# Performance work log

Hardware: AMD Instinct MI355X
Metric: run time of the kernel (lower is better)

## Reference

```python
import jax, jax.numpy as jnp
import numpy as np

B, T, N = 4096, 96, 32
E, K, D_MODEL = 4, 2, 32
PATCHES = (8, 6, 4, 12)
DECOMP_KERNELS = (4, 8, 12)
FOURIER_TOPK = 3
NOISE_EPS = 0.01
LOSS_COEF = 1e-4
SQRT2 = float(np.sqrt(2.0))


def _moving_avg(x, k):
    # x: (B, T, N); replicate-pad so output length stays T (stride-1 avg pool)
    pl, pr = (k - 1) // 2, k // 2
    xp = jnp.concatenate([jnp.repeat(x[:, :1], pl, axis=1), x,
                          jnp.repeat(x[:, -1:], pr, axis=1)], axis=1)
    c = jnp.cumsum(xp, axis=1)
    c = jnp.concatenate([jnp.zeros_like(c[:, :1]), c], axis=1)
    return (c[:, k:] - c[:, :-k]) / k


def _fourier_seasonality(x, topk=FOURIER_TOPK):
    # keep top-k amplitude non-DC frequencies per (batch, node) series
    f = jnp.fft.rfft(x, axis=1)                       # (B, F, N)
    amp = jnp.abs(f).at[:, 0].set(0.0)
    kth = -jnp.sort(-amp, axis=1)[:, topk - 1:topk]   # k-th largest amplitude
    mask = (amp >= kth).astype(f.dtype)
    return jnp.fft.irfft(f * mask, n=x.shape[1], axis=1)


def _cv_squared(v):
    return jnp.var(v, ddof=1) / (jnp.mean(v) ** 2 + 1e-10)


def _prob_in_top_k(clean, noisy, std, top_vals, k):
    # top_vals: (B, k+1) descending noisy top values
    std = jnp.maximum(std, 1e-6)
    thr_in = top_vals[:, k:k + 1]        # (k+1)-th value -> threshold if sample is in
    thr_out = top_vals[:, k - 1:k]       # k-th value -> threshold if sample is out
    z_in = jnp.clip((clean - thr_in) / std, -50.0, 50.0)
    z_out = jnp.clip((clean - thr_out) / std, -50.0, 50.0)
    p_in = jnp.clip(0.5 * (1.0 + jax.lax.erf(z_in / SQRT2)), 0.0, 1.0)
    p_out = jnp.clip(0.5 * (1.0 + jax.lax.erf(z_out / SQRT2)), 0.0, 1.0)
    return jnp.where(noisy > thr_in, p_in, p_out)


def _patch_expert(x2, p, w1, b1, w2, b2):
    # per-expert patch MLP: split T into patches of size p, mix within patch
    Bb, Tt, Nn = x2.shape
    xr = x2.reshape(Bb, Tt // p, p, Nn).transpose(0, 1, 3, 2)  # (B, Pn, N, p)
    h = jax.nn.gelu(xr @ w1 + b1)                               # (B, Pn, N, d)
    y = h @ w2 + b2                                             # (B, Pn, N, p)
    return y.transpose(0, 1, 3, 2).reshape(Bb, Tt, Nn)


def _forward(x, noise, w_start, b_start, wg, bg, wn, bn, eparams):
    x2 = x[..., 0]                                              # (B, T, N)
    trend = jnp.mean(jnp.stack([_moving_avg(x2, k) for k in DECOMP_KERNELS]), axis=0)
    season = _fourier_seasonality(x2)
    new_x = x2 + season + trend

    # ---- noisy top-k gating ----
    x_lin = new_x @ w_start + b_start                           # (B, T)
    clean = x_lin @ wg.T + bg                                   # (B, E)
    std = jnp.clip(jax.nn.softplus(x_lin @ wn.T + bn) + NOISE_EPS, 1e-3, 1e3)
    noisy = clean + noise * std
    top_vals, top_idx = jax.lax.top_k(noisy, K + 1)
    gk = jax.nn.softmax(top_vals[:, :K], axis=1)
    rows = jnp.arange(noisy.shape[0])[:, None]
    gates = jnp.zeros_like(noisy).at[rows, top_idx[:, :K]].set(gk)  # (B, E) sparse

    prob = _prob_in_top_k(clean, noisy, std, top_vals, K)
    load = prob.sum(0)
    importance = gates.sum(0)
    balance_loss = (_cv_squared(importance) + _cv_squared(load)) * LOSS_COEF

    # ---- dispatch / expert / combine (dense weighted form; gate==0 rows vanish,
    # same math as SparseDispatcher gather + weighted scatter-add) ----
    out = jnp.zeros_like(x2)
    for i, p in enumerate(PATCHES):
        w1, b1, w2, b2 = eparams[i]
        y = _patch_expert(x2, p, w1, b1, w2, b2)
        out = out + gates[:, i][:, None, None] * y
    return out[..., None], balance_loss


def setup_inputs() -> dict:
    key = jax.random.key(0)
    ks = jax.random.split(key, 32)
    inp = {
        "x": jax.random.normal(ks[0], (B, T, N, 1), jnp.float32),
        "noise": jax.random.normal(ks[1], (B, E), jnp.float32),
        "w_start": 0.1 * jax.random.normal(ks[2], (N,), jnp.float32),
        "b_start": jnp.zeros((1,), jnp.float32),
        "wg": 0.05 * jax.random.normal(ks[3], (E, T), jnp.float32),
        "bg": jnp.zeros((E,), jnp.float32),
        "wn": 0.05 * jax.random.normal(ks[4], (E, T), jnp.float32),
        "bn": jnp.zeros((E,), jnp.float32),
    }
    for i, p in enumerate(PATCHES):
        inp[f"e{i}_w1"] = 0.1 * jax.random.normal(ks[5 + 2 * i], (p, D_MODEL), jnp.float32)
        inp[f"e{i}_b1"] = jnp.zeros((D_MODEL,), jnp.float32)
        inp[f"e{i}_w2"] = 0.1 * jax.random.normal(ks[6 + 2 * i], (D_MODEL, p), jnp.float32)
        inp[f"e{i}_b2"] = jnp.zeros((p,), jnp.float32)
    return inp


def reference(x, noise, w_start, b_start, wg, bg, wn, bn,
              e0_w1, e0_b1, e0_w2, e0_b2,
              e1_w1, e1_b1, e1_w2, e1_b2,
              e2_w1, e2_b1, e2_w2, e2_b2,
              e3_w1, e3_b1, e3_w2, e3_b2):
    eparams = ((e0_w1, e0_b1, e0_w2, e0_b2),
               (e1_w1, e1_b1, e1_w2, e1_b2),
               (e2_w1, e2_b1, e2_w2, e2_b2),
               (e3_w1, e3_b1, e3_w2, e3_b2))
    return _forward(x, noise, w_start, b_start, wg, bg, wn, bn, eparams)
```

## Files before the change

kernel.cpp:

```cpp
#include <hip/hip_runtime.h>
#include <math.h>

#define NTHREADS 256
constexpr int TB = 4096;
constexpr int TT = 96;
constexpr int TN = 32;
constexpr int XLD = 33;

struct Params {
    const float* x; const float* noise;
    const float* w_start; const float* b_start;
    const float* wg; const float* bg; const float* wn; const float* bn;
    const float* ew[16];
    float* out; float* part;
};

__device__ __forceinline__ float gelu_f(float v) {
    float v2 = v * v;
    float u2 = fmaf(0.0713548162726278f * v, v2, 1.5957691216057308f * v);
    float t = __expf(-u2);
    return v * __builtin_amdgcn_rcpf(1.0f + t);
}

template<int P, int L0, int L1, int CB>
__device__ __forceinline__ void patch_acc2(const float* __restrict__ xg,
        const float* __restrict__ w1, const float* __restrict__ w2,
        const float* __restrict__ b1, const float* __restrict__ b2,
        int pbA, int pbB, int n, float g, float (&yA)[12], float (&yB)[12]) {
    float vA[P], vB[P];
    #pragma unroll
    for (int l = 0; l < P; ++l) {
        vA[l] = xg[(pbA * P + l) * TN + n];
        vB[l] = xg[(pbB * P + l) * TN + n];
    }
    #pragma unroll 2
    for (int jb = 0; jb < 8; ++jb) {
        float aA0 = b1[jb * 4 + 0], aA1 = b1[jb * 4 + 1];
        float aA2 = b1[jb * 4 + 2], aA3 = b1[jb * 4 + 3];
        float aB0 = aA0, aB1 = aA1, aB2 = aA2, aB3 = aA3;
        #pragma unroll
        for (int l = 0; l < P; ++l) {
            const float w0 = w1[l * 32 + jb * 4 + 0];
            const float w1v = w1[l * 32 + jb * 4 + 1];
            const float w2v = w1[l * 32 + jb * 4 + 2];
            const float w3 = w1[l * 32 + jb * 4 + 3];
            aA0 = fmaf(vA[l], w0, aA0);  aA1 = fmaf(vA[l], w1v, aA1);
            aA2 = fmaf(vA[l], w2v, aA2); aA3 = fmaf(vA[l], w3, aA3);
            aB0 = fmaf(vB[l], w0, aB0);  aB1 = fmaf(vB[l], w1v, aB1);
            aB2 = fmaf(vB[l], w2v, aB2); aB3 = fmaf(vB[l], w3, aB3);
        }
        float hA[4], hB[4];
        hA[0] = g * gelu_f(aA0); hA[1] = g * gelu_f(aA1);
        hA[2] = g * gelu_f(aA2); hA[3] = g * gelu_f(aA3);
        hB[0] = g * gelu_f(aB0); hB[1] = g * gelu_f(aB1);
        hB[2] = g * gelu_f(aB2); hB[3] = g * gelu_f(aB3);
        #pragma unroll
        for (int l = L0; l < L1; ++l) {
            float accA = yA[CB + l - L0];
            float accB = yB[CB + l - L0];
            #pragma unroll
            for (int q = 0; q < 4; ++q) {
                const float w = w2[(jb * 4 + q) * P + l];
                accA = fmaf(hA[q], w, accA);
                accB = fmaf(hB[q], w, accB);
            }
            yA[CB + l - L0] = accA;
            yB[CB + l - L0] = accB;
        }
    }
    #pragma unroll
    for (int l = L0; l < L1; ++l) {
        yA[CB + l - L0] = fmaf(g, b2[l], yA[CB + l - L0]);
        yB[CB + l - L0] = fmaf(g, b2[l], yB[CB + l - L0]);
    }
}

__global__ __launch_bounds__(NTHREADS) void ams_k1(Params p) {
    __shared__ float xs[TT * XLD];
    __shared__ float ct[96], st[96];
    __shared__ float xlin[96];
    __shared__ float selr[256], seli[256];
    __shared__ int   selk[256];
    __shared__ int   selcnt[32];
    __shared__ float wst[32];
    __shared__ float gtmp[8];
    __shared__ float b0sh;

    const int tid = threadIdx.x;
    const int b = blockIdx.x;

    const float* xb = p.x + (size_t)b * (TT * TN);
    #pragma unroll 1
    for (int idx = tid; idx < TT * TN; idx += NTHREADS)
        xs[(idx >> 5) * XLD + (idx & 31)] = xb[idx];
    if (tid < 96) {
        float ang = (float)tid * 0.06544984694978735f;
        ct[tid] = cosf(ang);
        st[tid] = sinf(ang);
    }
    if (tid < 32) wst[tid] = p.w_start[tid];
    if (tid == 0) b0sh = p.b_start[0];
    __syncthreads();

    {
        const int n = tid >> 3;
        const int kslot = tid & 7;
        const int lane = tid & 63;

        float Sr[12], Si[12];
        #pragma unroll
        for (int bb = 0; bb < 12; ++bb) { Sr[bb] = 0.0f; Si[bb] = 0.0f; }
        {
            const int step = 12 * kslot;
            int idx8 = 0;
            #pragma unroll 2
            for (int a = 0; a < 8; ++a) {
                float c8 = ct[idx8], s8 = st[idx8];
                idx8 += step; idx8 = (idx8 >= 96) ? idx8 - 96 : idx8;
                const float* xrow = &xs[(12 * a) * XLD + n];
                #pragma unroll
                for (int bb = 0; bb < 12; ++bb) {
                    float xv = xrow[bb * XLD];
                    Sr[bb] = fmaf(xv, c8, Sr[bb]);
                    Si[bb] = fmaf(xv, s8, Si[bb]);
                }
            }
        }

        float ar[7], ai[7];
        #pragma unroll
        for (int u = 0; u < 7; ++u) {
            const int k = kslot + 8 * u;
            const float ckv = ct[k];
            const float skv = st[k];
            float cb = 1.0f, sb = 0.0f, arx = 0.0f, aix = 0.0f;
            #pragma unroll
            for (int bb = 0; bb < 12; ++bb) {
                arx = fmaf(cb, Sr[bb], arx);
                arx = fmaf(-sb, Si[bb], arx);
                aix = fmaf(cb, Si[bb], aix);
                aix = fmaf(sb, Sr[bb], aix);
                float cn = fmaf(cb, ckv, -(sb * skv));
                float sn = fmaf(sb, ckv,  cb * skv);
                cb = cn; sb = sn;
            }
            ar[u] = arx; ai[u] = aix;
        }

        float amp[7];
        #pragma unroll
        for (int u = 0; u < 7; ++u) {
            int k = kslot + 8 * u;
            amp[u] = (k == 0) ? 0.0f : ((k <= 48) ? sqrtf(ar[u] * ar[u] + ai[u] * ai[u]) : -1.0f);
        }
        float v1 = -2.0f, v2 = -2.0f, v3 = -2.0f;
        #pragma unroll
        for (int u = 0; u < 7; ++u) {
            float a = amp[u];
            if (a > v1)      { v3 = v2; v2 = v1; v1 = a; }
            else if (a > v2) { v3 = v2; v2 = a; }
            else if (a > v3) { v3 = a; }
        }
        #pragma unroll
        for (int d = 1; d <= 4; d <<= 1) {
            float b1v = __shfl_xor(v1, d, 64);
            float b2v = __shfl_xor(v2, d, 64);
            float b3v = __shfl_xor(v3, d, 64);
            float m1 = fmaxf(v1, b1v), n1 = fminf(v1, b1v);
            float m2 = fmaxf(v2, b2v), n2 = fminf(v2, b2v);
            float s3 = (v1 > b1v) ? v3 : b3v;
            float c3 = fmaxf(fmaxf(fminf(n1, m2), n2), s3);
            v2 = fmaxf(n1, m2);
            v1 = m1;
            v3 = c3;
        }
        int qc = 0;
        #pragma unroll
        for (int u = 0; u < 7; ++u) qc += (amp[u] >= v3) ? 1 : 0;
        int inc = qc;
        #pragma unroll
        for (int d = 1; d <= 4; d <<= 1) {
            int t = __shfl_up(inc, d, 64);
            if (kslot >= d) inc += t;
        }
        int off = inc - qc;
        int cnt = __shfl(inc, lane | 7, 64);
        if (kslot == 0) selcnt[n] = (cnt < 8) ? cnt : 8;
        int w = off;
        #pragma unroll
        for (int u = 0; u < 7; ++u) {
            int k = kslot + 8 * u;
            if (amp[u] >= v3 && w < 8) {
                float wgt = (k == 0 || k == 48) ? (1.0f / 96.0f) : (2.0f / 96.0f);
                selk[w * 32 + n] = k;
                selr[w * 32 + n] = wgt * ar[u];
                seli[w * 32 + n] = wgt * ai[u];
                w++;
            }
        }
    }
    __syncthreads();

    {
        float b0 = b0sh;
        const int t0 = tid >> 5;
        const int n  = tid & 31;
        const int cnt = selcnt[n];
        float A0 = 0, B0 = 0, c0 = 1, s0 = 0, c80 = 1, s80 = 0;
        float A1 = 0, B1 = 0, c1 = 1, s1 = 0, c81 = 1, s81 = 0;
        float A2 = 0, B2 = 0, c2 = 1, s2 = 0, c82 = 1, s82 = 0;
        #define SETROT(Q, A, B, C, S, C8, S8) \
            if (Q < cnt) { \
                int k = selk[Q * 32 + n]; \
                A = selr[Q * 32 + n]; B = seli[Q * 32 + n]; \
                int m0 = (t0 * k) % 96; C = ct[m0]; S = st[m0]; \
                int m8 = (8 * k) % 96;  C8 = ct[m8]; S8 = st[m8]; \
            }
        SETROT(0, A0, B0, c0, s0, c80, s80)
        SETROT(1, A1, B1, c1, s1, c81, s81)
        SETROT(2, A2, B2, c2, s2, c82, s82)
        #undef SETROT
        #pragma unroll 1
        for (int j = 0; j < 12; ++j) {
            int t = t0 + 8 * j;
            float xv = xs[t * XLD + n];
            #define XC(tt) xs[(((tt) < 0) ? 0 : (((tt) > 95) ? 95 : (tt))) * XLD + n]
            float s4  = XC(t - 1) + xv + XC(t + 1) + XC(t + 2);
            float s8  = s4  + XC(t - 3) + XC(t - 2) + XC(t + 3) + XC(t + 4);
            float s12 = s8  + XC(t - 5) + XC(t - 4) + XC(t + 5) + XC(t + 6);
            #undef XC
            float trend = (s4 * 0.25f + s8 * 0.125f + s12 * (1.0f / 12.0f)) * (1.0f / 3.0f);
            float season = A0 * c0 + B0 * s0 + A1 * c1 + B1 * s1 + A2 * c2 + B2 * s2;
            float nc0 = fmaf(c0, c80, -(s0 * s80)), ns0 = fmaf(s0, c80, c0 * s80);
            float nc1 = fmaf(c1, c81, -(s1 * s81)), ns1 = fmaf(s1, c81, c1 * s81);
            float nc2 = fmaf(c2, c82, -(s2 * s82)), ns2 = fmaf(s2, c82, c2 * s82);
            c0 = nc0; s0 = ns0; c1 = nc1; s1 = ns1; c2 = nc2; s2 = ns2;
            #pragma unroll 1
            for (int q = 3; q < cnt; ++q) {
                int k = selk[q * 32 + n];
                int m = (t * k) % 96;
                season = fmaf(selr[q * 32 + n], ct[m], season);
                season = fmaf(seli[q * 32 + n], st[m], season);
            }
            float val = (xv + trend + season) * wst[n];
            #pragma unroll
            for (int d = 16; d >= 1; d >>= 1) val += __shfl_xor(val, d, 64);
            if ((tid & 31) == 0) xlin[t] = val + b0;
        }
    }
    __syncthreads();

    {
        int e8 = tid >> 5;
        int tl = tid & 31;
        int eb = e8 & 3;
        const float* W = ((e8 < 4) ? p.wg : p.wn) + eb * 96;
        float acc = 0.0f;
        #pragma unroll
        for (int c = 0; c < 3; ++c)
            acc = fmaf(xlin[tl + 32 * c], W[tl + 32 * c], acc);
        #pragma unroll
        for (int d = 16; d >= 1; d >>= 1) acc += __shfl_xor(acc, d, 64);
        if (tl == 0) gtmp[e8] = acc + ((e8 < 4) ? p.bg[eb] : p.bn[eb]);
    }
    __syncthreads();
    if (tid == 0) {
        float clean[4], stdv[4], noisy[4];
        #pragma unroll
        for (int e = 0; e < 4; ++e) {
            clean[e] = gtmp[e];
            float r = gtmp[4 + e];
            float sp = fmaxf(r, 0.0f) + log1pf(expf(-fabsf(r)));
            stdv[e] = fminf(fmaxf(sp + 0.01f, 0.001f), 1000.0f);
            noisy[e] = clean[e] + p.noise[(size_t)b * 4 + e] * stdv[e];
        }
        int i1 = 0, i2 = -1;
        float v1 = -INFINITY, v2 = -INFINITY, v3 = -INFINITY;
        for (int e = 0; e < 4; ++e) if (noisy[e] > v1) { v1 = noisy[e]; i1 = e; }
        for (int e = 0; e < 4; ++e) if (e != i1 && noisy[e] > v2) { v2 = noisy[e]; i2 = e; }
        for (int e = 0; e < 4; ++e) if (e != i1 && e != i2 && noisy[e] > v3) { v3 = noisy[e]; }
        float e2 = expf(v2 - v1);
        float g1 = 1.0f / (1.0f + e2);
        float g2 = e2 * g1;
        float gates[4] = {0.0f, 0.0f, 0.0f, 0.0f};
        gates[i1] = g1; gates[i2] = g2;
        const float inv_sqrt2 = 0.7071067811865476f;
        #pragma unroll
        for (int e = 0; e < 4; ++e) {
            float thr = (noisy[e] > v3) ? v3 : v2;
            float z = (clean[e] - thr) / stdv[e];
            z = fminf(fmaxf(z, -50.0f), 50.0f);
            float pr = 0.5f * (1.0f + erff(z * inv_sqrt2));
            pr = fminf(fmaxf(pr, 0.0f), 1.0f);
            p.part[(size_t)b * 8 + e] = gates[e];
            p.part[(size_t)b * 8 + 4 + e] = pr;
        }
    }
}

__global__ __launch_bounds__(NTHREADS) void ams_k2(Params p) {
    const int tid = threadIdx.x;
    const int half = tid >> 7;
    const size_t b = 2 * (size_t)blockIdx.x + half;
    const int g = tid & 127;
    const int cA = ((g >> 5) & 1) * 2 + (g >> 6);
    const int cB = cA + 4;
    const int n = g & 31;

    const float g0 = p.part[b * 8 + 0];
    const float g1 = p.part[b * 8 + 1];
    const float g2 = p.part[b * 8 + 2];
    const float g3 = p.part[b * 8 + 3];
    const float* xg = p.x + b * (TT * TN);

    float yA[12], yB[12];
    #pragma unroll
    for (int r = 0; r < 12; ++r) { yA[r] = 0.0f; yB[r] = 0.0f; }

    if (g0 != 0.0f) {
        if (cA & 1) {
            int pb = (3 * cA - 1) >> 1;
            patch_acc2<8, 4, 8, 0>(xg, p.ew[0], p.ew[2], p.ew[1], p.ew[3], pb,     pb + 6, n, g0, yA, yB);
            patch_acc2<8, 0, 8, 4>(xg, p.ew[0], p.ew[2], p.ew[1], p.ew[3], pb + 1, pb + 7, n, g0, yA, yB);
        } else {
            int pb = (3 * cA) >> 1;
            patch_acc2<8, 0, 8, 0>(xg, p.ew[0], p.ew[2], p.ew[1], p.ew[3], pb,     pb + 6, n, g0, yA, yB);
            patch_acc2<8, 0, 4, 8>(xg, p.ew[0], p.ew[2], p.ew[1], p.ew[3], pb + 1, pb + 7, n, g0, yA, yB);
        }
    }
    if (g1 != 0.0f) {
        patch_acc2<6, 0, 6, 0>(xg, p.ew[4], p.ew[6], p.ew[5], p.ew[7], 2 * cA,     2 * cA + 8, n, g1, yA, yB);
        patch_acc2<6, 0, 6, 6>(xg, p.ew[4], p.ew[6], p.ew[5], p.ew[7], 2 * cA + 1, 2 * cA + 9, n, g1, yA, yB);
    }
    if (g2 != 0.0f) {
        patch_acc2<4, 0, 4, 0>(xg, p.ew[8], p.ew[10], p.ew[9], p.ew[11], 3 * cA,     3 * cA + 12, n, g2, yA, yB);
        patch_acc2<4, 0, 4, 4>(xg, p.ew[8], p.ew[10], p.ew[9], p.ew[11], 3 * cA + 1, 3 * cA + 13, n, g2, yA, yB);
        patch_acc2<4, 0, 4, 8>(xg, p.ew[8], p.ew[10], p.ew[9], p.ew[11], 3 * cA + 2, 3 * cA + 14, n, g2, yA, yB);
    }
    if (g3 != 0.0f) {
        patch_acc2<12, 0, 12, 0>(xg, p.ew[12], p.ew[14], p.ew[13], p.ew[15], cA, cB, n, g3, yA, yB);
    }

    float* ob = p.out + b * (TT * TN);
    float* obA = ob + (size_t)(12 * cA) * 32 + n;
    float* obB = ob + (size_t)(12 * cB) * 32 + n;
    #pragma unroll
    for (int r = 0; r < 12; ++r) {
        obA[r * 32] = yA[r];
        obB[r * 32] = yB[r];
    }
}

__global__ __launch_bounds__(NTHREADS) void ams_finalize(const float* __restrict__ part,
                                                         float* __restrict__ out_loss) {
    __shared__ float red[4][8];
    float acc[8] = {0, 0, 0, 0, 0, 0, 0, 0};
    #pragma unroll 1
    for (int r = threadIdx.x; r < TB; r += NTHREADS) {
        #pragma unroll
        for (int c = 0; c < 8; ++c) acc[c] += part[(size_t)r * 8 + c];
    }
    #pragma unroll
    for (int c = 0; c < 8; ++c) {
        #pragma unroll
        for (int d = 32; d >= 1; d >>= 1) acc[c] += __shfl_xor(acc[c], d, 64);
    }
    int wid = threadIdx.x >> 6;
    if ((threadIdx.x & 63) == 0) {
        #pragma unroll
        for (int c = 0; c < 8; ++c) red[wid][c] = acc[c];
    }
    __syncthreads();
    if (threadIdx.x == 0) {
        float imp[4], load[4];
        #pragma unroll
        for (int c = 0; c < 4; ++c) imp[c]  = red[0][c] + red[1][c] + red[2][c] + red[3][c];
        #pragma unroll
        for (int c = 0; c < 4; ++c) load[c] = red[0][4 + c] + red[1][4 + c] + red[2][4 + c] + red[3][4 + c];
        float mi = (imp[0] + imp[1] + imp[2] + imp[3]) * 0.25f;
        float vi = 0.0f;
        #pragma unroll
        for (int i = 0; i < 4; ++i) { float d = imp[i] - mi; vi += d * d; }
        vi *= (1.0f / 3.0f);
        float ml = (load[0] + load[1] + load[2] + load[3]) * 0.25f;
        float vl = 0.0f;
        #pragma unroll
        for (int i = 0; i < 4; ++i) { float d = load[i] - ml; vl += d * d; }
        vl *= (1.0f / 3.0f);
        float cvi = vi / (mi * mi + 1e-10f);
        float cvl = vl / (ml * ml + 1e-10f);
        out_loss[0] = (cvi + cvl) * 1e-4f;
    }
}

extern "C" void kernel_launch(void* const* d_in, const int* in_sizes, int n_in,
                              void* d_out, int out_size, void* d_ws, size_t ws_size,
                              hipStream_t stream) {
    Params p;
    p.x       = (const float*)d_in[0];
    p.noise   = (const float*)d_in[1];
    p.w_start = (const float*)d_in[2];
    p.b_start = (const float*)d_in[3];
    p.wg      = (const float*)d_in[4];
    p.bg      = (const float*)d_in[5];
    p.wn      = (const float*)d_in[6];
    p.bn      = (const float*)d_in[7];
    for (int i = 0; i < 16; ++i) p.ew[i] = (const float*)d_in[8 + i];
    p.out  = (float*)d_out;
    p.part = (float*)d_ws;

    ams_k1<<<TB, NTHREADS, 0, stream>>>(p);
    ams_k2<<<TB / 2, NTHREADS, 0, stream>>>(p);
    ams_finalize<<<1, NTHREADS, 0, stream>>>((const float*)d_ws,
                                             (float*)d_out + (size_t)TB * TT * TN);
}
```

Measured before the change: 163.7 us.

## Give each k2 thread two 24-step time chunks, loading inputs once into registers

ams_k2 now maps one wavefront per batch row, and each thread owns two 24-step time chunks for one node. 24 is a common multiple of all patch sizes, so every expert's patches line up with chunk boundaries. Each thread loads its 48 input values into registers once and reuses them across all experts. This drops the redundant global loads and the odd/even branching on partial patches. In exchange it doubles per-thread work and register use (48 inputs plus 48 accumulators) and halves the number of threads, which may lower occupancy.

```diff
diff --git a/kernel.cpp b/kernel.cpp
--- a/kernel.cpp
+++ b/kernel.cpp
@@ -22,17 +22,11 @@
     return v * __builtin_amdgcn_rcpf(1.0f + t);
 }
 
-template<int P, int L0, int L1, int CB>
-__device__ __forceinline__ void patch_acc2(const float* __restrict__ xg,
+template<int P, int X0>
+__device__ __forceinline__ void patchF(const float (&x0)[24], const float (&x1)[24],
         const float* __restrict__ w1, const float* __restrict__ w2,
         const float* __restrict__ b1, const float* __restrict__ b2,
-        int pbA, int pbB, int n, float g, float (&yA)[12], float (&yB)[12]) {
-    float vA[P], vB[P];
-    #pragma unroll
-    for (int l = 0; l < P; ++l) {
-        vA[l] = xg[(pbA * P + l) * TN + n];
-        vB[l] = xg[(pbB * P + l) * TN + n];
-    }
+        float g, float (&y0)[24], float (&y1)[24]) {
     #pragma unroll 2
     for (int jb = 0; jb < 8; ++jb) {
         float aA0 = b1[jb * 4 + 0], aA1 = b1[jb * 4 + 1];
@@ -40,14 +34,16 @@
         float aB0 = aA0, aB1 = aA1, aB2 = aA2, aB3 = aA3;
         #pragma unroll
         for (int l = 0; l < P; ++l) {
+            const float vA = x0[X0 + l];
+            const float vB = x1[X0 + l];
             const float w0 = w1[l * 32 + jb * 4 + 0];
             const float w1v = w1[l * 32 + jb * 4 + 1];
             const float w2v = w1[l * 32 + jb * 4 + 2];
             const float w3 = w1[l * 32 + jb * 4 + 3];
-            aA0 = fmaf(vA[l], w0, aA0);  aA1 = fmaf(vA[l], w1v, aA1);
-            aA2 = fmaf(vA[l], w2v, aA2); aA3 = fmaf(vA[l], w3, aA3);
-            aB0 = fmaf(vB[l], w0, aB0);  aB1 = fmaf(vB[l], w1v, aB1);
-            aB2 = fmaf(vB[l], w2v, aB2); aB3 = fmaf(vB[l], w3, aB3);
+            aA0 = fmaf(vA, w0, aA0);  aA1 = fmaf(vA, w1v, aA1);
+            aA2 = fmaf(vA, w2v, aA2); aA3 = fmaf(vA, w3, aA3);
+            aB0 = fmaf(vB, w0, aB0);  aB1 = fmaf(vB, w1v, aB1);
+            aB2 = fmaf(vB, w2v, aB2); aB3 = fmaf(vB, w3, aB3);
         }
         float hA[4], hB[4];
         hA[0] = g * gelu_f(aA0); hA[1] = g * gelu_f(aA1);
@@ -55,23 +51,23 @@
         hB[0] = g * gelu_f(aB0); hB[1] = g * gelu_f(aB1);
         hB[2] = g * gelu_f(aB2); hB[3] = g * gelu_f(aB3);
         #pragma unroll
-        for (int l = L0; l < L1; ++l) {
-            float accA = yA[CB + l - L0];
-            float accB = yB[CB + l - L0];
+        for (int l = 0; l < P; ++l) {
+            float accA = y0[X0 + l];
+            float accB = y1[X0 + l];
             #pragma unroll
             for (int q = 0; q < 4; ++q) {
                 const float w = w2[(jb * 4 + q) * P + l];
                 accA = fmaf(hA[q], w, accA);
                 accB = fmaf(hB[q], w, accB);
             }
-            yA[CB + l - L0] = accA;
-            yB[CB + l - L0] = accB;
+            y0[X0 + l] = accA;
+            y1[X0 + l] = accB;
         }
     }
     #pragma unroll
-    for (int l = L0; l < L1; ++l) {
-        yA[CB + l - L0] = fmaf(g, b2[l], yA[CB + l - L0]);
-        yB[CB + l - L0] = fmaf(g, b2[l], yB[CB + l - L0]);
+    for (int l = 0; l < P; ++l) {
+        y0[X0 + l] = fmaf(g, b2[l], y0[X0 + l]);
+        y1[X0 + l] = fmaf(g, b2[l], y1[X0 + l]);
     }
 }
 
@@ -300,12 +296,10 @@
 
 __global__ __launch_bounds__(NTHREADS) void ams_k2(Params p) {
     const int tid = threadIdx.x;
-    const int half = tid >> 7;
-    const size_t b = 2 * (size_t)blockIdx.x + half;
-    const int g = tid & 127;
-    const int cA = ((g >> 5) & 1) * 2 + (g >> 6);
-    const int cB = cA + 4;
-    const int n = g & 31;
+    const size_t b = 4 * (size_t)blockIdx.x + (tid >> 6);
+    const int lane = tid & 63;
+    const int hi = lane >> 5;
+    const int n = lane & 31;
 
     const float g0 = p.part[b * 8 + 0];
     const float g1 = p.part[b * 8 + 1];
@@ -313,41 +307,51 @@
     const float g3 = p.part[b * 8 + 3];
     const float* xg = p.x + b * (TT * TN);
 
-    float yA[12], yB[12];
+    float x0[24], x1[24];
+    {
+        const float* p0 = xg + (24 * hi) * TN + n;
+        const float* p1 = xg + (24 * hi + 48) * TN + n;
+        #pragma unroll
+        for (int r = 0; r < 24; ++r) {
+            x0[r] = p0[r * TN];
+            x1[r] = p1[r * TN];
+        }
+    }
+
+    float y0[24], y1[24];
     #pragma unroll
-    for (int r = 0; r < 12; ++r) { yA[r] = 0.0f; yB[r] = 0.0f; }
+    for (int r = 0; r < 24; ++r) { y0[r] = 0.0f; y1[r] = 0.0f; }
 
     if (g0 != 0.0f) {
-        if (cA & 1) {
-            int pb = (3 * cA - 1) >> 1;
-            patch_acc2<8, 4, 8, 0>(xg, p.ew[0], p.ew[2], p.ew[1], p.ew[3], pb,     pb + 6, n, g0, yA, yB);
-            patch_acc2<8, 0, 8, 4>(xg, p.ew[0], p.ew[2], p.ew[1], p.ew[3], pb + 1, pb + 7, n, g0, yA, yB);
-        } else {
-            int pb = (3 * cA) >> 1;
-            patch_acc2<8, 0, 8, 0>(xg, p.ew[0], p.ew[2], p.ew[1], p.ew[3], pb,     pb + 6, n, g0, yA, yB);
-            patch_acc2<8, 0, 4, 8>(xg, p.ew[0], p.ew[2], p.ew[1], p.ew[3], pb + 1, pb + 7, n, g0, yA, yB);
-        }
+        patchF<8, 0>(x0, x1, p.ew[0], p.ew[2], p.ew[1], p.ew[3], g0, y0, y1);
+        patchF<8, 8>(x0, x1, p.ew[0], p.ew[2], p.ew[1], p.ew[3], g0, y0, y1);
+        patchF<8, 16>(x0, x1, p.ew[0], p.ew[2], p.ew[1], p.ew[3], g0, y0, y1);
     }
     if (g1 != 0.0f) {
-        patch_acc2<6, 0, 6, 0>(xg, p.ew[4], p.ew[6], p.ew[5], p.ew[7], 2 * cA,     2 * cA + 8, n, g1, yA, yB);
-        patch_acc2<6, 0, 6, 6>(xg, p.ew[4], p.ew[6], p.ew[5], p.ew[7], 2 * cA + 1, 2 * cA + 9, n, g1, yA, yB);
+        patchF<6, 0>(x0, x1, p.ew[4], p.ew[6], p.ew[5], p.ew[7], g1, y0, y1);
+        patchF<6, 6>(x0, x1, p.ew[4], p.ew[6], p.ew[5], p.ew[7], g1, y0, y1);
+        patchF<6, 12>(x0, x1, p.ew[4], p.ew[6], p.ew[5], p.ew[7], g1, y0, y1);
+        patchF<6, 18>(x0, x1, p.ew[4], p.ew[6], p.ew[5], p.ew[7], g1, y0, y1);
     }
     if (g2 != 0.0f) {
-        patch_acc2<4, 0, 4, 0>(xg, p.ew[8], p.ew[10], p.ew[9], p.ew[11], 3 * cA,     3 * cA + 12, n, g2, yA, yB);
-        patch_acc2<4, 0, 4, 4>(xg, p.ew[8], p.ew[10], p.ew[9], p.ew[11], 3 * cA + 1, 3 * cA + 13, n, g2, yA, yB);
-        patch_acc2<4, 0, 4, 8>(xg, p.ew[8], p.ew[10], p.ew[9], p.ew[11], 3 * cA + 2, 3 * cA + 14, n, g2, yA, yB);
+        patchF<4, 0>(x0, x1, p.ew[8], p.ew[10], p.ew[9], p.ew[11], g2, y0, y1);
+        patchF<4, 4>(x0, x1, p.ew[8], p.ew[10], p.ew[9], p.ew[11], g2, y0, y1);
+        patchF<4, 8>(x0, x1, p.ew[8], p.ew[10], p.ew[9], p.ew[11], g2, y0, y1);
+        patchF<4, 12>(x0, x1, p.ew[8], p.ew[10], p.ew[9], p.ew[11], g2, y0, y1);
+        patchF<4, 16>(x0, x1, p.ew[8], p.ew[10], p.ew[9], p.ew[11], g2, y0, y1);
+        patchF<4, 20>(x0, x1, p.ew[8], p.ew[10], p.ew[9], p.ew[11], g2, y0, y1);
     }
     if (g3 != 0.0f) {
-        patch_acc2<12, 0, 12, 0>(xg, p.ew[12], p.ew[14], p.ew[13], p.ew[15], cA, cB, n, g3, yA, yB);
-    }
-
-    float* ob = p.out + b * (TT * TN);
-    float* obA = ob + (size_t)(12 * cA) * 32 + n;
-    float* obB = ob + (size_t)(12 * cB) * 32 + n;
+        patchF<12, 0>(x0, x1, p.ew[12], p.ew[14], p.ew[13], p.ew[15], g3, y0, y1);
+        patchF<12, 12>(x0, x1, p.ew[12], p.ew[14], p.ew[13], p.ew[15], g3, y0, y1);
+    }
+
+    float* o0 = p.out + b * (TT * TN) + (size_t)(24 * hi) * 32 + n;
+    float* o1 = o0 + 48 * 32;
     #pragma unroll
-    for (int r = 0; r < 12; ++r) {
-        obA[r * 32] = yA[r];
-        obB[r * 32] = yB[r];
+    for (int r = 0; r < 24; ++r) {
+        o0[r * 32] = y0[r];
+        o1[r * 32] = y1[r];
     }
 }
 
@@ -410,7 +414,7 @@
     p.part = (float*)d_ws;
 
     ams_k1<<<TB, NTHREADS, 0, stream>>>(p);
-    ams_k2<<<TB / 2, NTHREADS, 0, stream>>>(p);
+    ams_k2<<<TB / 4, NTHREADS, 0, stream>>>(p);
     ams_finalize<<<1, NTHREADS, 0, stream>>>((const float*)d_ws,
                                              (float*)d_out + (size_t)TB * TT * TN);
 }
```

After: 174.3 us. +6.4%, slower.
